# Optimization experiments

Hardware: AMD Instinct MI355X
Metric: run time of the kernel (lower is better)

Reference implementation:

```python
import jax, jax.numpy as jnp
import numpy as np

N_NODES = 50000
N_EDGES = 800000
IN_DIM = 128
OUT_DIM = 128
NUM_EDGE_TYPES = 16
RULE_FEAT_DIM = 4


def setup_inputs() -> dict:
    key = jax.random.key(0)
    ks = jax.random.split(key, 20)
    d = OUT_DIM
    s_in = 1.0 / np.sqrt(IN_DIM)
    s_d = 1.0 / np.sqrt(d)
    s_r = 1.0 / np.sqrt(RULE_FEAT_DIM)
    inp = {
        "x": jax.random.normal(ks[0], (N_NODES, IN_DIM), jnp.float32),
        "edge_index": jax.random.randint(ks[1], (2, N_EDGES), 0, N_NODES),
        "edge_type": jax.random.randint(ks[2], (N_EDGES,), 0, NUM_EDGE_TYPES),
        "edge_rule_feat": jax.random.normal(ks[3], (N_EDGES, RULE_FEAT_DIM), jnp.float32),
        "total_nodes": N_NODES,
        # parameters (Linear stored as [in, out]; y = x @ W + b)
        "Wq": jax.random.uniform(ks[4], (IN_DIM, d), jnp.float32, -s_in, s_in),
        "bq": jnp.zeros((d,), jnp.float32),
        "Wk": jax.random.uniform(ks[5], (IN_DIM, d), jnp.float32, -s_in, s_in),
        "bk": jnp.zeros((d,), jnp.float32),
        "Wv": jax.random.uniform(ks[6], (IN_DIM, d), jnp.float32, -s_in, s_in),
        "bv": jnp.zeros((d,), jnp.float32),
        "rel_emb": jax.random.normal(ks[7], (NUM_EDGE_TYPES, d), jnp.float32),
        "attn_vec": jax.random.normal(ks[8], (3 * d,), jnp.float32),
        "rule_w1": jax.random.uniform(ks[9], (RULE_FEAT_DIM, d), jnp.float32, -s_r, s_r),
        "rule_b1": jnp.zeros((d,), jnp.float32),
        "rule_w2": jax.random.uniform(ks[10], (d, 1), jnp.float32, -s_d, s_d),
        "rule_b2": jnp.zeros((1,), jnp.float32),  # zero-initialized in source
        "gate_rule_w": jax.random.uniform(ks[11], (RULE_FEAT_DIM, 1), jnp.float32, -s_r, s_r),
        "gate_rule_b": jnp.zeros((1,), jnp.float32),
        "gate_neural_w": jax.random.uniform(ks[12], (2 * d, 1), jnp.float32, -1.0 / np.sqrt(2 * d), 1.0 / np.sqrt(2 * d)),
        "gate_neural_b": jnp.zeros((1,), jnp.float32),
        "msg_w": jax.random.uniform(ks[13], (d, d), jnp.float32, -s_d, s_d),
        "msg_b": jnp.zeros((d,), jnp.float32),
    }
    return inp


def reference(x, edge_index, edge_type, edge_rule_feat, total_nodes,
              Wq, bq, Wk, bk, Wv, bv, rel_emb, attn_vec,
              rule_w1, rule_b1, rule_w2, rule_b2,
              gate_rule_w, gate_rule_b, gate_neural_w, gate_neural_b,
              msg_w, msg_b):
    src, dst = edge_index[0], edge_index[1]
    d = msg_w.shape[0]

    h_src = x[src] @ Wk + bk                  # [E, d]
    h_dst = x[dst] @ Wq + bq                  # [E, d]
    rel = rel_emb[edge_type]                  # [E, d]

    # (cat([h_src,h_dst,rel]) * attn_vec).sum(-1) without materializing the concat
    a1, a2, a3 = attn_vec[:d], attn_vec[d:2 * d], attn_vec[2 * d:]
    e_base = jax.nn.leaky_relu(h_src @ a1 + h_dst @ a2 + rel @ a3, negative_slope=0.2)

    hidden = jax.nn.relu(edge_rule_feat @ rule_w1 + rule_b1)
    b_ij = (hidden @ rule_w2)[:, 0] + rule_b2[0]          # rule bias per edge

    gate_logit = (edge_rule_feat @ gate_rule_w)[:, 0] + gate_rule_b[0] \
               + (h_src @ gate_neural_w[:d, 0] + h_dst @ gate_neural_w[d:, 0]) + gate_neural_b[0]
    gamma_ij = jax.nn.sigmoid(gate_logit)

    e = e_base + gamma_ij * b_ij

    n = total_nodes
    # segment softmax over dst (numerically stable)
    seg_max = jax.ops.segment_max(e, dst, num_segments=n)
    e_exp = jnp.exp(e - seg_max[dst])
    seg_sum = jax.ops.segment_sum(e_exp, dst, num_segments=n)
    alpha = e_exp / (seg_sum[dst] + 1e-16)

    # eval mode: dropout is identity
    msg = ((x[src] @ Wv + bv + rel) @ msg_w + msg_b) * alpha[:, None]
    out = jax.ops.segment_sum(msg, dst, num_segments=n)   # index_add over dst
    return out, alpha, gamma_ij, b_ij
```

## Files before the change

kernel.cpp:

```cpp
#include <hip/hip_runtime.h>
#include <math.h>


using bf16x8 = __attribute__((ext_vector_type(8))) short;
using f32x4  = __attribute__((ext_vector_type(4))) float;

__device__ __forceinline__ float wave_max(float v) {
    #pragma unroll
    for (int o = 32; o > 0; o >>= 1) v = fmaxf(v, __shfl_xor(v, o, 64));
    return v;
}
__device__ __forceinline__ float wave_sum(float v) {
    #pragma unroll
    for (int o = 32; o > 0; o >>= 1) v += __shfl_xor(v, o, 64);
    return v;
}

__device__ __forceinline__ unsigned bf16rne(float f) {
    unsigned u = __float_as_uint(f);
    return (u + 0x7FFFu + ((u >> 16) & 1u)) >> 16;
}
__device__ __forceinline__ float bflo(unsigned u) { return __uint_as_float(u << 16); }
__device__ __forceinline__ float bfhi(unsigned u) { return __uint_as_float(u & 0xFFFF0000u); }

__global__ void __launch_bounds__(128) precompute_kernel(
    const float* __restrict__ Wq, const float* __restrict__ bq,
    const float* __restrict__ Wk, const float* __restrict__ bk,
    const float* __restrict__ Wv, const float* __restrict__ bv,
    const float* __restrict__ rel_emb, const float* __restrict__ attn_vec,
    const float* __restrict__ msg_w, const float* __restrict__ msg_b,
    const float* __restrict__ gnw, const float* __restrict__ grb,
    const float* __restrict__ gnb,
    const float* __restrict__ rule_w1, const float* __restrict__ rule_b1,
    const float* __restrict__ rule_w2,
    unsigned short* __restrict__ W2bT, float* __restrict__ c2,
    float* __restrict__ wkA, float* __restrict__ wqA,
    float* __restrict__ wkG, float* __restrict__ wqG,
    float* __restrict__ relA, float* __restrict__ relM,
    float* __restrict__ consts,
    float4* __restrict__ w1t, float2* __restrict__ w12)
{
    __shared__ float red[128];
    int bid = blockIdx.x, j = threadIdx.x;

    auto blk_reduce = [&](float v) -> float {
        red[j] = v;
        __syncthreads();
        for (int s = 64; s > 0; s >>= 1) {
            if (j < s) red[j] += red[j + s];
            __syncthreads();
        }
        float r = red[0];
        __syncthreads();
        return r;
    };

    if (bid < 128) {
        int i = bid;
        float acc = 0.f;
        #pragma unroll 8
        for (int k = 0; k < 128; ++k) acc = fmaf(Wv[i * 128 + k], msg_w[k * 128 + j], acc);
        W2bT[j * 128 + i] = (unsigned short)bf16rne(acc);
        float r;
        r = blk_reduce(Wk[i * 128 + j] * attn_vec[j]);        if (j == 0) wkA[i] = r;
        r = blk_reduce(Wq[i * 128 + j] * attn_vec[128 + j]);  if (j == 0) wqA[i] = r;
        r = blk_reduce(Wk[i * 128 + j] * gnw[j]);             if (j == 0) wkG[i] = r;
        r = blk_reduce(Wq[i * 128 + j] * gnw[128 + j]);       if (j == 0) wqG[i] = r;
    } else if (bid < 144) {
        int t = bid - 128;
        float acc = 0.f;
        #pragma unroll 8
        for (int k = 0; k < 128; ++k) acc = fmaf(rel_emb[t * 128 + k], msg_w[k * 128 + j], acc);
        relM[t * 128 + j] = acc;
        float r = blk_reduce(rel_emb[t * 128 + j] * attn_vec[256 + j]);
        if (j == 0) relA[t] = r;
    } else if (bid == 144) {
        float acc = msg_b[j];
        #pragma unroll 8
        for (int k = 0; k < 128; ++k) acc = fmaf(bv[k], msg_w[k * 128 + j], acc);
        c2[j] = acc;
        w1t[j] = make_float4(rule_w1[j], rule_w1[128 + j], rule_w1[256 + j], rule_w1[384 + j]);
        w12[j] = make_float2(rule_b1[j], rule_w2[j]);
    } else {
        float r = blk_reduce(bk[j] * attn_vec[j] + bq[j] * attn_vec[128 + j]);
        if (j == 0) consts[0] = r;
        r = blk_reduce(bk[j] * gnw[j] + bq[j] * gnw[128 + j]);
        if (j == 0) consts[1] = r + grb[0] + gnb[0];
    }
}

__global__ void __launch_bounds__(256) node_kernel(
    const float4* __restrict__ x4, const unsigned short* __restrict__ W2bT,
    const float* __restrict__ c2,
    const float* __restrict__ wkA, const float* __restrict__ wqA,
    const float* __restrict__ wkG, const float* __restrict__ wqG,
    unsigned* __restrict__ Vmb, float2* __restrict__ srcPack,
    float2* __restrict__ dstPack, int* __restrict__ deg, int n_nodes)
{
    __shared__ unsigned short Asu[128][136];
    __shared__ unsigned short Bsu[128][136];
    const int tid = threadIdx.x;
    const int rowBase = blockIdx.x * 128;

    if (tid < 128 && rowBase + tid < n_nodes) deg[rowBase + tid] = 0;

    #pragma unroll
    for (int l = 0; l < 16; ++l) {
        int flat = l * 256 + tid;
        int r = flat >> 5, k4 = flat & 31;
        int row = rowBase + r;
        float4 v = (row < n_nodes) ? x4[row * 32 + k4] : make_float4(0.f, 0.f, 0.f, 0.f);
        uint2 u;
        u.x = bf16rne(v.x) | (bf16rne(v.y) << 16);
        u.y = bf16rne(v.z) | (bf16rne(v.w) << 16);
        *(uint2*)&Asu[r][k4 * 4] = u;
    }
    #pragma unroll
    for (int l = 0; l < 16; ++l) {
        int flat = l * 256 + tid;
        int n = flat >> 5, kq = flat & 31;
        uint2 w = *(const uint2*)&W2bT[n * 128 + kq * 4];
        *(uint2*)&Bsu[n][kq * 4] = w;
    }

    {
        int r = tid & 127, h = tid >> 7;
        int row = rowBase + r;
        if (row < n_nodes) {
            const float4* wa4 = (const float4*)(h ? wqA : wkA);
            const float4* wg4 = (const float4*)(h ? wqG : wkG);
            float sA = 0.f, sG = 0.f;
            #pragma unroll 8
            for (int k4 = 0; k4 < 32; ++k4) {
                float4 xv = x4[row * 32 + k4];
                float4 wa = wa4[k4], wg = wg4[k4];
                sA = fmaf(xv.x, wa.x, fmaf(xv.y, wa.y, fmaf(xv.z, wa.z, fmaf(xv.w, wa.w, sA))));
                sG = fmaf(xv.x, wg.x, fmaf(xv.y, wg.y, fmaf(xv.z, wg.z, fmaf(xv.w, wg.w, sG))));
            }
            if (h) dstPack[row] = make_float2(sA, sG);
            else   srcPack[row] = make_float2(sA, sG);
        }
    }
    __syncthreads();

    const int wave = tid >> 6, lane = tid & 63;
    const int ln = lane & 15, quad = lane >> 4;
    const int wm = (wave & 1) * 64, wn = (wave >> 1) * 64;

    f32x4 acc[4][4];
    #pragma unroll
    for (int i = 0; i < 4; ++i)
        #pragma unroll
        for (int j = 0; j < 4; ++j) acc[i][j] = (f32x4){0.f, 0.f, 0.f, 0.f};

    #pragma unroll
    for (int kc = 0; kc < 4; ++kc) {
        int k0 = kc * 32 + quad * 8;
        bf16x8 afr[4], bfr[4];
        #pragma unroll
        for (int mt = 0; mt < 4; ++mt)
            afr[mt] = *(const bf16x8*)&Asu[wm + mt * 16 + ln][k0];
        #pragma unroll
        for (int nt = 0; nt < 4; ++nt)
            bfr[nt] = *(const bf16x8*)&Bsu[wn + nt * 16 + ln][k0];
        #pragma unroll
        for (int mt = 0; mt < 4; ++mt)
            #pragma unroll
            for (int nt = 0; nt < 4; ++nt)
                acc[mt][nt] = __builtin_amdgcn_mfma_f32_16x16x32_bf16(
                    afr[mt], bfr[nt], acc[mt][nt], 0, 0, 0);
    }

    #pragma unroll
    for (int nt = 0; nt < 4; ++nt) {
        int col = wn + nt * 16 + ln;
        float cb = c2[col];
        #pragma unroll
        for (int mt = 0; mt < 4; ++mt) {
            #pragma unroll
            for (int r = 0; r < 4; ++r) {
                int row = rowBase + wm + mt * 16 + quad * 4 + r;
                float v = acc[mt][nt][r] + cb;
                float pv = __shfl_xor(v, 1, 64);
                if (!(ln & 1) && row < n_nodes) {
                    Vmb[row * 64 + (col >> 1)] = bf16rne(v) | (bf16rne(pv) << 16);
                }
            }
        }
    }
}

__global__ void __launch_bounds__(256) edge1a_kernel(
    const float4* __restrict__ erf,
    const float4* __restrict__ w1t, const float2* __restrict__ w12,
    const float* __restrict__ rule_b2,
    float* __restrict__ b_out, int n_edges)
{
    __shared__ float4 s_w1t[128];
    __shared__ float2 s_w12[128];
    const int tid = threadIdx.x;
    if (tid < 128) { s_w1t[tid] = w1t[tid]; s_w12[tid] = w12[tid]; }
    __syncthreads();

    const int eb = blockIdx.x * 1024;
    float4 rf[4];
    #pragma unroll
    for (int q = 0; q < 4; ++q) {
        int e = eb + q * 256 + tid;
        rf[q] = erf[min(e, n_edges - 1)];
    }

    float bacc[4] = {0.f, 0.f, 0.f, 0.f};
    #pragma unroll 2
    for (int j = 0; j < 128; ++j) {
        float4 w = s_w1t[j];
        float2 c = s_w12[j];
        #pragma unroll
        for (int q = 0; q < 4; ++q) {
            float h = fmaf(rf[q].x, w.x, fmaf(rf[q].y, w.y,
                      fmaf(rf[q].z, w.z, fmaf(rf[q].w, w.w, c.x))));
            bacc[q] = fmaf(fmaxf(h, 0.f), c.y, bacc[q]);
        }
    }

    const float rb2 = rule_b2[0];
    #pragma unroll
    for (int q = 0; q < 4; ++q) {
        int e = eb + q * 256 + tid;
        if (e < n_edges) b_out[e] = bacc[q] + rb2;
    }
}

__global__ void __launch_bounds__(256) edge1b_kernel(
    const int* __restrict__ ei, const int* __restrict__ et,
    const float4* __restrict__ erf, const float* __restrict__ grw,
    const float2* __restrict__ srcPack, const float2* __restrict__ dstPack,
    const float* __restrict__ relA, const float* __restrict__ consts,
    const float* __restrict__ b_out,
    float* __restrict__ e_val, float* __restrict__ gamma_out,
    int* __restrict__ deg, int n_edges)
{
    int e = blockIdx.x * 256 + threadIdx.x;
    if (e >= n_edges) return;

    int s = ei[e], d = ei[n_edges + e], t = et[e];
    float4 rf = erf[e];
    float b = b_out[e];
    float2 ss = srcPack[s], dd = dstPack[d];

    float pre = ss.x + dd.x + relA[t] + consts[0];
    float e_base = pre >= 0.f ? pre : 0.2f * pre;

    float gl = fmaf(rf.x, grw[0], fmaf(rf.y, grw[1],
               fmaf(rf.z, grw[2], fmaf(rf.w, grw[3], consts[1] + ss.y + dd.y))));
    float gamma = 1.f / (1.f + __expf(-gl));

    gamma_out[e] = gamma;
    e_val[e] = e_base + gamma * b;
    atomicAdd(&deg[d], 1);
}

__global__ void __launch_bounds__(256) scan1_kernel(
    const int* __restrict__ deg, int* __restrict__ rowPtr,
    int* __restrict__ partials, int n)
{
    __shared__ int sdata[256];
    int tid = threadIdx.x;
    int base = blockIdx.x * 1024 + tid * 4;
    int v0 = (base + 0 < n) ? deg[base + 0] : 0;
    int v1 = (base + 1 < n) ? deg[base + 1] : 0;
    int v2 = (base + 2 < n) ? deg[base + 2] : 0;
    int v3 = (base + 3 < n) ? deg[base + 3] : 0;
    int tsum = v0 + v1 + v2 + v3;
    sdata[tid] = tsum;
    __syncthreads();
    #pragma unroll
    for (int off = 1; off < 256; off <<= 1) {
        int t = (tid >= off) ? sdata[tid - off] : 0;
        __syncthreads();
        sdata[tid] += t;
        __syncthreads();
    }
    int excl = sdata[tid] - tsum;
    if (base + 0 < n) rowPtr[base + 0] = excl;
    if (base + 1 < n) rowPtr[base + 1] = excl + v0;
    if (base + 2 < n) rowPtr[base + 2] = excl + v0 + v1;
    if (base + 3 < n) rowPtr[base + 3] = excl + v0 + v1 + v2;
    if (tid == 255) partials[blockIdx.x] = sdata[255];
}

__global__ void __launch_bounds__(64) scan2_kernel(int* __restrict__ partials, int nb)
{
    int lane = threadIdx.x;
    int v = (lane < nb) ? partials[lane] : 0;
    int orig = v;
    #pragma unroll
    for (int off = 1; off < 64; off <<= 1) {
        int t = __shfl_up(v, off, 64);
        if (lane >= off) v += t;
    }
    if (lane < nb) partials[lane] = v - orig;
}

__global__ void __launch_bounds__(256) scan3_kernel(
    int* __restrict__ rowPtr, const int* __restrict__ partials,
    int* __restrict__ bucketCursor, int n, int n_edges)
{
    int off = partials[blockIdx.x];
    int base = blockIdx.x * 1024 + threadIdx.x * 4;
    #pragma unroll
    for (int k = 0; k < 4; ++k) {
        int idx = base + k;
        if (idx < n) {
            int r = rowPtr[idx] + off;
            rowPtr[idx] = r;
            if ((idx & 255) == 0) bucketCursor[idx >> 8] = r;
        }
    }
    if (blockIdx.x == 0 && threadIdx.x == 0) rowPtr[n] = n_edges;
}

__global__ void __launch_bounds__(256) sort1_kernel(
    const int* __restrict__ ei, const int* __restrict__ et,
    const float* __restrict__ e_val, int* __restrict__ bucketCursor,
    float2* __restrict__ tmp, int n_edges)
{
    __shared__ float2 data[4096];
    __shared__ unsigned char slotB[4096];
    __shared__ int cnt[256], rk[256], base_[256], run[256], scanBuf[256];
    const int tid = threadIdx.x;
    const int blockBase = blockIdx.x * 4096;
    const int total = min(4096, n_edges - blockBase);

    cnt[tid] = 0;
    rk[tid] = 0;
    __syncthreads();

    int   d_[16];
    float ev_[16];
    int   pk_[16];
    #pragma unroll
    for (int i = 0; i < 16; ++i) {
        int e = blockBase + i * 256 + tid;
        if (e < n_edges) {
            int d = ei[n_edges + e];
            d_[i]  = d;
            ev_[i] = e_val[e];
            pk_[i] = (ei[e] & 0xFFFF) | ((et[e] & 15) << 16) | ((d & 255) << 20);
            atomicAdd(&cnt[d >> 8], 1);
        } else {
            d_[i] = -1;
        }
    }
    __syncthreads();

    int c = cnt[tid];
    scanBuf[tid] = c;
    __syncthreads();
    #pragma unroll
    for (int off = 1; off < 256; off <<= 1) {
        int t = (tid >= off) ? scanBuf[tid - off] : 0;
        __syncthreads();
        scanBuf[tid] += t;
        __syncthreads();
    }
    base_[tid] = scanBuf[tid] - c;
    run[tid] = c ? atomicAdd(&bucketCursor[tid], c) : 0;
    __syncthreads();

    #pragma unroll
    for (int i = 0; i < 16; ++i) {
        if (d_[i] >= 0) {
            int b = d_[i] >> 8;
            int r = atomicAdd(&rk[b], 1);
            int slot = base_[b] + r;
            data[slot] = make_float2(ev_[i], __int_as_float(pk_[i]));
            slotB[slot] = (unsigned char)b;
        }
    }
    __syncthreads();

    for (int j = tid; j < total; j += 256) {
        int b = slotB[j];
        tmp[run[b] + (j - base_[b])] = data[j];
    }
}

__global__ void __launch_bounds__(256) sort2_kernel(
    const int* __restrict__ rowPtr, const float2* __restrict__ tmp,
    float2* __restrict__ payload, int n_nodes)
{
    __shared__ int cur[256];
    const int tid = threadIdx.x;
    const int d0 = blockIdx.x * 256;
    const int dEnd = min(d0 + 256, n_nodes);
    if (d0 + tid < dEnd) cur[tid] = rowPtr[d0 + tid];
    __syncthreads();
    const int lo = rowPtr[d0];
    const int hi = rowPtr[dEnd];
    for (int j = lo + tid; j < hi; j += 256) {
        float2 p = tmp[j];
        unsigned pk = __float_as_uint(p.y);
        int dl = (pk >> 20) & 255;
        int pos = atomicAdd(&cur[dl], 1);
        unsigned st = (pk & 0xFFFFu) | (((pk >> 16) & 15u) << 27);
        payload[pos] = make_float2(p.x, __uint_as_float(st));
    }
}

__global__ void __launch_bounds__(256) gather_kernel(
    const int* __restrict__ rowPtr, const float2* __restrict__ payload,
    const unsigned* __restrict__ Vmb, const float* __restrict__ relM,
    float* __restrict__ out, float2* __restrict__ nodeMS, int n_nodes)
{
    __shared__ float2 s_relM[16 * 64];
    const int tid = threadIdx.x;
    const float2* relM2 = (const float2*)relM;
    #pragma unroll
    for (int i = 0; i < 4; ++i) s_relM[i * 256 + tid] = relM2[i * 256 + tid];
    __syncthreads();

    int lane = tid & 63;
    int d = blockIdx.x * 4 + (tid >> 6);
    if (d >= n_nodes) return;
    int start = rowPtr[d];
    int deg = rowPtr[d + 1] - start;

    float acc0 = 0.f, acc1 = 0.f;
    float m = -INFINITY, inv;

    auto acc8 = [&](float av, int st, int k) {
        float a[8];
        int s[8];
        #pragma unroll
        for (int i = 0; i < 8; ++i) {
            a[i] = __shfl(av, k + i, 64);
            s[i] = __shfl(st, k + i, 64);
        }
        unsigned v[8];
        float2 rm[8];
        #pragma unroll
        for (int i = 0; i < 8; ++i) {
            int ss = s[i] & 0x7FFFFFF;
            int tt = ((unsigned)s[i]) >> 27;
            v[i]  = Vmb[ss * 64 + lane];
            rm[i] = s_relM[tt * 64 + lane];
        }
        #pragma unroll
        for (int i = 0; i < 8; ++i) {
            acc0 = fmaf(a[i], bflo(v[i]) + rm[i].x, acc0);
            acc1 = fmaf(a[i], bfhi(v[i]) + rm[i].y, acc1);
        }
    };

    if (deg <= 64) {
        float ev = -INFINITY;
        int st = 0;
        if (lane < deg) {
            float2 p = payload[start + lane];
            ev = p.x;
            st = __float_as_int(p.y);
        }
        m = wave_max(ev);
        float ex = (lane < deg) ? __expf(ev - m) : 0.f;
        float sum = wave_sum(ex);
        inv = 1.f / (sum + 1e-16f);
        float av = ex * inv;
        for (int k = 0; k < deg; k += 8) acc8(av, st, k);
    } else {
        for (int i = lane; i < deg; i += 64) m = fmaxf(m, payload[start + i].x);
        m = wave_max(m);
        float sum = 0.f;
        for (int i = lane; i < deg; i += 64) sum += __expf(payload[start + i].x - m);
        sum = wave_sum(sum);
        inv = 1.f / (sum + 1e-16f);
        for (int c = 0; c < deg; c += 64) {
            int i = c + lane;
            float av = 0.f;
            int st = 0;
            if (i < deg) {
                float2 p = payload[start + i];
                av = __expf(p.x - m) * inv;
                st = __float_as_int(p.y);
            }
            int cnt = min(64, deg - c);
            for (int k = 0; k < cnt; k += 8) acc8(av, st, k);
        }
    }
    if (lane == 0) nodeMS[d] = make_float2(m, inv);
    *(float2*)&out[d * 128 + lane * 2] = make_float2(acc0, acc1);
}

__global__ void __launch_bounds__(256) alpha_kernel(
    const int* __restrict__ ei, const float* __restrict__ e_val,
    const float2* __restrict__ nodeMS, float* __restrict__ alpha_out, int n_edges)
{
    int e = blockIdx.x * blockDim.x + threadIdx.x;
    if (e >= n_edges) return;
    int d = ei[n_edges + e];
    float2 ms = nodeMS[d];
    alpha_out[e] = __expf(e_val[e] - ms.x) * ms.y;
}

extern "C" void kernel_launch(void* const* d_in, const int* in_sizes, int n_in,
                              void* d_out, int out_size, void* d_ws, size_t ws_size,
                              hipStream_t stream)
{
    const float* x        = (const float*)d_in[0];
    const int*   ei       = (const int*)d_in[1];
    const int*   et       = (const int*)d_in[2];
    const float* erf      = (const float*)d_in[3];
    const float* Wq       = (const float*)d_in[5];
    const float* bq       = (const float*)d_in[6];
    const float* Wk       = (const float*)d_in[7];
    const float* bk       = (const float*)d_in[8];
    const float* Wv       = (const float*)d_in[9];
    const float* bv       = (const float*)d_in[10];
    const float* rel_emb  = (const float*)d_in[11];
    const float* attn_vec = (const float*)d_in[12];
    const float* rule_w1  = (const float*)d_in[13];
    const float* rule_b1  = (const float*)d_in[14];
    const float* rule_w2  = (const float*)d_in[15];
    const float* rule_b2  = (const float*)d_in[16];
    const float* grw      = (const float*)d_in[17];
    const float* grb      = (const float*)d_in[18];
    const float* gnw      = (const float*)d_in[19];
    const float* gnb      = (const float*)d_in[20];
    const float* msg_w    = (const float*)d_in[21];
    const float* msg_b    = (const float*)d_in[22];

    const int n_nodes = in_sizes[0] / 128;
    const int n_edges = in_sizes[2];
    const int nb = (n_nodes + 1023) / 1024;
    const int nbuck = (n_nodes + 255) / 256;

    float* ws = (float*)d_ws;
    size_t off = 0;
    unsigned* Vmb  = (unsigned*)(ws + off); off += (size_t)n_nodes * 64;
    float2* payload = (float2*)(ws + off); off += 2 * (size_t)n_edges;
    float2* tmpPay  = (float2*)(ws + off); off += 2 * (size_t)n_edges;
    float* e_val   = ws + off; off += n_edges;
    float* srcPack = ws + off; off += 2 * (size_t)n_nodes;
    float* dstPack = ws + off; off += 2 * (size_t)n_nodes;
    float2* nodeMS = (float2*)(ws + off); off += 2 * (size_t)n_nodes;
    int*   deg     = (int*)(ws + off); off += n_nodes;
    int*   rowPtr  = (int*)(ws + off); off += n_nodes + 4;
    int*   partials= (int*)(ws + off); off += 64;
    int*   bucketCursor = (int*)(ws + off); off += 256;
    unsigned short* W2bT = (unsigned short*)(ws + off); off += 128 * 64;
    float* c2      = ws + off; off += 128;
    float* wkA     = ws + off; off += 128;
    float* wqA     = ws + off; off += 128;
    float* wkG     = ws + off; off += 128;
    float* wqG     = ws + off; off += 128;
    float* relA    = ws + off; off += 16;
    float* relM    = ws + off; off += 16 * 128;
    float* consts  = ws + off; off += 2;
    off += 2;
    float4* w1t    = (float4*)(ws + off); off += 128 * 4;
    float2* w12    = (float2*)(ws + off); off += 128 * 2;

    float* out       = (float*)d_out;
    float* alpha_out = out + (size_t)n_nodes * 128;
    float* gamma_out = alpha_out + n_edges;
    float* b_out     = gamma_out + n_edges;

    hipLaunchKernelGGL(precompute_kernel, dim3(146), dim3(128), 0, stream,
                       Wq, bq, Wk, bk, Wv, bv, rel_emb, attn_vec, msg_w, msg_b,
                       gnw, grb, gnb, rule_w1, rule_b1, rule_w2,
                       W2bT, c2, wkA, wqA, wkG, wqG, relA, relM, consts, w1t, w12);

    hipLaunchKernelGGL(node_kernel, dim3((n_nodes + 127) / 128), dim3(256), 0, stream,
                       (const float4*)x, W2bT, c2,
                       wkA, wqA, wkG, wqG, Vmb, (float2*)srcPack, (float2*)dstPack,
                       deg, n_nodes);

    hipLaunchKernelGGL(edge1a_kernel, dim3((n_edges + 1023) / 1024), dim3(256), 0, stream,
                       (const float4*)erf, (const float4*)w1t, (const float2*)w12,
                       rule_b2, b_out, n_edges);

    hipLaunchKernelGGL(edge1b_kernel, dim3((n_edges + 255) / 256), dim3(256), 0, stream,
                       ei, et, (const float4*)erf, grw,
                       (const float2*)srcPack, (const float2*)dstPack,
                       relA, consts, b_out, e_val, gamma_out, deg, n_edges);

    hipLaunchKernelGGL(scan1_kernel, dim3(nb), dim3(256), 0, stream,
                       deg, rowPtr, partials, n_nodes);
    hipLaunchKernelGGL(scan2_kernel, dim3(1), dim3(64), 0, stream,
                       partials, nb);
    hipLaunchKernelGGL(scan3_kernel, dim3(nb), dim3(256), 0, stream,
                       rowPtr, partials, bucketCursor, n_nodes, n_edges);

    hipLaunchKernelGGL(sort1_kernel, dim3((n_edges + 4095) / 4096), dim3(256), 0, stream,
                       ei, et, e_val, bucketCursor, tmpPay, n_edges);

    hipLaunchKernelGGL(sort2_kernel, dim3(nbuck), dim3(256), 0, stream,
                       rowPtr, tmpPay, payload, n_nodes);

    hipLaunchKernelGGL(gather_kernel, dim3((n_nodes + 3) / 4), dim3(256), 0, stream,
                       rowPtr, payload, Vmb, relM, out, nodeMS, n_nodes);

    hipLaunchKernelGGL(alpha_kernel, dim3((n_edges + 255) / 256), dim3(256), 0, stream,
                       ei, e_val, nodeMS, alpha_out, n_edges);
}
```

Measured before the change: 296.4 us.

## Replace per-node degree atomics and 3-pass scan with bucket histogram

```diff
diff --git a/kernel.cpp b/kernel.cpp
--- a/kernel.cpp
+++ b/kernel.cpp
@@ -95,14 +95,12 @@
     const float* __restrict__ wkA, const float* __restrict__ wqA,
     const float* __restrict__ wkG, const float* __restrict__ wqG,
     unsigned* __restrict__ Vmb, float2* __restrict__ srcPack,
-    float2* __restrict__ dstPack, int* __restrict__ deg, int n_nodes)
+    float2* __restrict__ dstPack, int n_nodes)
 {
     __shared__ unsigned short Asu[128][136];
     __shared__ unsigned short Bsu[128][136];
     const int tid = threadIdx.x;
     const int rowBase = blockIdx.x * 128;
-
-    if (tid < 128 && rowBase + tid < n_nodes) deg[rowBase + tid] = 0;
 
     #pragma unroll
     for (int l = 0; l < 16; ++l) {
@@ -238,7 +236,7 @@
     const float* __restrict__ relA, const float* __restrict__ consts,
     const float* __restrict__ b_out,
     float* __restrict__ e_val, float* __restrict__ gamma_out,
-    int* __restrict__ deg, int n_edges)
+    int n_edges)
 {
     int e = blockIdx.x * 256 + threadIdx.x;
     if (e >= n_edges) return;
@@ -257,22 +255,33 @@
 
     gamma_out[e] = gamma;
     e_val[e] = e_base + gamma * b;
-    atomicAdd(&deg[d], 1);
-}
-
-__global__ void __launch_bounds__(256) scan1_kernel(
-    const int* __restrict__ deg, int* __restrict__ rowPtr,
-    int* __restrict__ partials, int n)
+}
+
+__global__ void __launch_bounds__(256) histo_kernel(
+    const int* __restrict__ dsts, int* __restrict__ hpart, int n_edges)
+{
+    __shared__ int cnt[256];
+    const int tid = threadIdx.x;
+    cnt[tid] = 0;
+    __syncthreads();
+    const int base = blockIdx.x * 4096;
+    const int end = min(base + 4096, n_edges);
+    for (int e = base + tid; e < end; e += 256)
+        atomicAdd(&cnt[dsts[e] >> 8], 1);
+    __syncthreads();
+    hpart[blockIdx.x * 256 + tid] = cnt[tid];
+}
+
+__global__ void __launch_bounds__(256) hscan_kernel(
+    const int* __restrict__ hpart, int* __restrict__ bucketCursor,
+    int* __restrict__ bucketStart, int* __restrict__ rowPtr,
+    int nblk, int n_nodes, int n_edges)
 {
     __shared__ int sdata[256];
-    int tid = threadIdx.x;
-    int base = blockIdx.x * 1024 + tid * 4;
-    int v0 = (base + 0 < n) ? deg[base + 0] : 0;
-    int v1 = (base + 1 < n) ? deg[base + 1] : 0;
-    int v2 = (base + 2 < n) ? deg[base + 2] : 0;
-    int v3 = (base + 3 < n) ? deg[base + 3] : 0;
-    int tsum = v0 + v1 + v2 + v3;
-    sdata[tid] = tsum;
+    const int tid = threadIdx.x;
+    int s = 0;
+    for (int i = 0; i < nblk; ++i) s += hpart[i * 256 + tid];
+    sdata[tid] = s;
     __syncthreads();
     #pragma unroll
     for (int off = 1; off < 256; off <<= 1) {
@@ -281,43 +290,10 @@
         sdata[tid] += t;
         __syncthreads();
     }
-    int excl = sdata[tid] - tsum;
-    if (base + 0 < n) rowPtr[base + 0] = excl;
-    if (base + 1 < n) rowPtr[base + 1] = excl + v0;
-    if (base + 2 < n) rowPtr[base + 2] = excl + v0 + v1;
-    if (base + 3 < n) rowPtr[base + 3] = excl + v0 + v1 + v2;
-    if (tid == 255) partials[blockIdx.x] = sdata[255];
-}
-
-__global__ void __launch_bounds__(64) scan2_kernel(int* __restrict__ partials, int nb)
-{
-    int lane = threadIdx.x;
-    int v = (lane < nb) ? partials[lane] : 0;
-    int orig = v;
-    #pragma unroll
-    for (int off = 1; off < 64; off <<= 1) {
-        int t = __shfl_up(v, off, 64);
-        if (lane >= off) v += t;
-    }
-    if (lane < nb) partials[lane] = v - orig;
-}
-
-__global__ void __launch_bounds__(256) scan3_kernel(
-    int* __restrict__ rowPtr, const int* __restrict__ partials,
-    int* __restrict__ bucketCursor, int n, int n_edges)
-{
-    int off = partials[blockIdx.x];
-    int base = blockIdx.x * 1024 + threadIdx.x * 4;
-    #pragma unroll
-    for (int k = 0; k < 4; ++k) {
-        int idx = base + k;
-        if (idx < n) {
-            int r = rowPtr[idx] + off;
-            rowPtr[idx] = r;
-            if ((idx & 255) == 0) bucketCursor[idx >> 8] = r;
-        }
-    }
-    if (blockIdx.x == 0 && threadIdx.x == 0) rowPtr[n] = n_edges;
+    int excl = sdata[tid] - s;
+    bucketCursor[tid] = excl;
+    bucketStart[tid] = excl;
+    if (tid == 0) rowPtr[n_nodes] = n_edges;
 }
 
 __global__ void __launch_bounds__(256) sort1_kernel(
@@ -387,17 +363,40 @@
 }
 
 __global__ void __launch_bounds__(256) sort2_kernel(
-    const int* __restrict__ rowPtr, const float2* __restrict__ tmp,
-    float2* __restrict__ payload, int n_nodes)
-{
-    __shared__ int cur[256];
+    const int* __restrict__ bucketStart, const float2* __restrict__ tmp,
+    float2* __restrict__ payload, int* __restrict__ rowPtr,
+    int n_nodes, int n_edges, int nbuck)
+{
+    __shared__ int cnt[256], cur[256], sdata[256];
     const int tid = threadIdx.x;
-    const int d0 = blockIdx.x * 256;
-    const int dEnd = min(d0 + 256, n_nodes);
-    if (d0 + tid < dEnd) cur[tid] = rowPtr[d0 + tid];
-    __syncthreads();
-    const int lo = rowPtr[d0];
-    const int hi = rowPtr[dEnd];
+    const int b = blockIdx.x;
+    const int d0 = b * 256;
+    const int lo = bucketStart[b];
+    const int hi = (b == nbuck - 1) ? n_edges : bucketStart[b + 1];
+
+    cnt[tid] = 0;
+    __syncthreads();
+    for (int j = lo + tid; j < hi; j += 256) {
+        unsigned pk = __float_as_uint(tmp[j].y);
+        atomicAdd(&cnt[(pk >> 20) & 255], 1);
+    }
+    __syncthreads();
+
+    int c = cnt[tid];
+    sdata[tid] = c;
+    __syncthreads();
+    #pragma unroll
+    for (int off = 1; off < 256; off <<= 1) {
+        int t = (tid >= off) ? sdata[tid - off] : 0;
+        __syncthreads();
+        sdata[tid] += t;
+        __syncthreads();
+    }
+    int excl = sdata[tid] - c;
+    cur[tid] = lo + excl;
+    if (d0 + tid < n_nodes) rowPtr[d0 + tid] = lo + excl;
+    __syncthreads();
+
     for (int j = lo + tid; j < hi; j += 256) {
         float2 p = tmp[j];
         unsigned pk = __float_as_uint(p.y);
@@ -531,7 +530,7 @@
 
     const int n_nodes = in_sizes[0] / 128;
     const int n_edges = in_sizes[2];
-    const int nb = (n_nodes + 1023) / 1024;
+    const int nhb = (n_edges + 4095) / 4096;
     const int nbuck = (n_nodes + 255) / 256;
 
     float* ws = (float*)d_ws;
@@ -543,10 +542,10 @@
     float* srcPack = ws + off; off += 2 * (size_t)n_nodes;
     float* dstPack = ws + off; off += 2 * (size_t)n_nodes;
     float2* nodeMS = (float2*)(ws + off); off += 2 * (size_t)n_nodes;
-    int*   deg     = (int*)(ws + off); off += n_nodes;
     int*   rowPtr  = (int*)(ws + off); off += n_nodes + 4;
-    int*   partials= (int*)(ws + off); off += 64;
+    int*   hpart   = (int*)(ws + off); off += (size_t)nhb * 256;
     int*   bucketCursor = (int*)(ws + off); off += 256;
+    int*   bucketStart  = (int*)(ws + off); off += 256;
     unsigned short* W2bT = (unsigned short*)(ws + off); off += 128 * 64;
     float* c2      = ws + off; off += 128;
     float* wkA     = ws + off; off += 128;
@@ -570,10 +569,17 @@
                        gnw, grb, gnb, rule_w1, rule_b1, rule_w2,
                        W2bT, c2, wkA, wqA, wkG, wqG, relA, relM, consts, w1t, w12);
 
+    hipLaunchKernelGGL(histo_kernel, dim3(nhb), dim3(256), 0, stream,
+                       ei + n_edges, hpart, n_edges);
+
+    hipLaunchKernelGGL(hscan_kernel, dim3(1), dim3(256), 0, stream,
+                       hpart, bucketCursor, bucketStart, rowPtr,
+                       nhb, n_nodes, n_edges);
+
     hipLaunchKernelGGL(node_kernel, dim3((n_nodes + 127) / 128), dim3(256), 0, stream,
                        (const float4*)x, W2bT, c2,
                        wkA, wqA, wkG, wqG, Vmb, (float2*)srcPack, (float2*)dstPack,
-                       deg, n_nodes);
+                       n_nodes);
 
     hipLaunchKernelGGL(edge1a_kernel, dim3((n_edges + 1023) / 1024), dim3(256), 0, stream,
                        (const float4*)erf, (const float4*)w1t, (const float2*)w12,
@@ -582,20 +588,14 @@
     hipLaunchKernelGGL(edge1b_kernel, dim3((n_edges + 255) / 256), dim3(256), 0, stream,
                        ei, et, (const float4*)erf, grw,
                        (const float2*)srcPack, (const float2*)dstPack,
-                       relA, consts, b_out, e_val, gamma_out, deg, n_edges);
-
-    hipLaunchKernelGGL(scan1_kernel, dim3(nb), dim3(256), 0, stream,
-                       deg, rowPtr, partials, n_nodes);
-    hipLaunchKernelGGL(scan2_kernel, dim3(1), dim3(64), 0, stream,
-                       partials, nb);
-    hipLaunchKernelGGL(scan3_kernel, dim3(nb), dim3(256), 0, stream,
-                       rowPtr, partials, bucketCursor, n_nodes, n_edges);
-
-    hipLaunchKernelGGL(sort1_kernel, dim3((n_edges + 4095) / 4096), dim3(256), 0, stream,
+                       relA, consts, b_out, e_val, gamma_out, n_edges);
+
+    hipLaunchKernelGGL(sort1_kernel, dim3(nhb), dim3(256), 0, stream,
                        ei, et, e_val, bucketCursor, tmpPay, n_edges);
 
     hipLaunchKernelGGL(sort2_kernel, dim3(nbuck), dim3(256), 0, stream,
-                       rowPtr, tmpPay, payload, n_nodes);
+                       bucketStart, tmpPay, payload, rowPtr,
+                       n_nodes, n_edges, nbuck);
 
     hipLaunchKernelGGL(gather_kernel, dim3((n_nodes + 3) / 4), dim3(256), 0, stream,
                        rowPtr, payload, Vmb, relM, out, nodeMS, n_nodes);
```

Measured after the change: 295.8 us. Within noise of the previous version (-0.2%).
